# Optimization experiments

Hardware: AMD Instinct MI355X
Metric: run time of the kernel (lower is better)

The kernel has to match this reference:

```python
import jax, jax.numpy as jnp
import numpy as np

B, M, P = 128, 35, 224  # batch, num Zernike modes, pupil_size
SIGN_PENALTY = 10.0
RECON_WEIGHT = 0.4
DEFOCUS_RAD = 1.0
EPS = 1e-8


def setup_inputs() -> dict:
    key = jax.random.key(0)
    k1, k2, k3, k4 = jax.random.split(key, 4)
    pred = jax.random.normal(k1, (B, M), dtype=jnp.float32)
    target = jax.random.normal(k2, (B, M), dtype=jnp.float32)
    input_psfs = jax.random.uniform(k3, (B, 2, P, P), dtype=jnp.float32)
    zernike_basis = jax.random.normal(k4, (M, P, P), dtype=jnp.float32)
    pupil_mask = jnp.ones((P, P), dtype=jnp.float32)
    return {
        "pred": pred,
        "target": target,
        "input_psfs": input_psfs,
        "zernike_basis": zernike_basis,
        "pupil_mask": pupil_mask,
    }


def _psf_from_phase(phase, pupil_mask):
    # phase: [B,P,P] real; pupil: masked complex field
    pupil = pupil_mask[None, :, :] * jnp.exp(1j * phase)
    field = jnp.fft.fftshift(jnp.fft.fft2(pupil), axes=(-2, -1))
    psf = field.real ** 2 + field.imag ** 2  # |FFT|^2
    psf = psf / (psf.sum(axis=(-2, -1), keepdims=True) + EPS)
    return psf


def reference(pred, target, input_psfs, zernike_basis, pupil_mask):
    # --- sign-weighted MSE on Zernike coefficients ---
    base = (pred - target) ** 2
    sign_match = jnp.sign(pred) * jnp.sign(target)
    weight = jnp.where(sign_match < 0, SIGN_PENALTY, 1.0)
    z_loss = jnp.mean(base * weight)

    # --- batched differentiable PSF reconstruction loss ---
    phase = jnp.einsum('bm,mhw->bhw', pred, zernike_basis)
    phase = phase * pupil_mask[None, :, :]

    sim_if = _psf_from_phase(phase, pupil_mask)  # in-focus

    lin = jnp.linspace(-1.0, 1.0, P, dtype=jnp.float32)
    y, x = jnp.meshgrid(lin, lin, indexing='ij')
    r2 = x ** 2 + y ** 2
    defocus_phase = DEFOCUS_RAD * (2.0 * r2 - 1.0)  # [P,P]
    sim_podf = _psf_from_phase(phase + defocus_phase[None, :, :], pupil_mask)

    # per-sample F.mse_loss then mean over batch == mean over the batched arrays
    recon_loss = (jnp.mean((sim_if - input_psfs[:, 0]) ** 2)
                  + jnp.mean((sim_podf - input_psfs[:, 1]) ** 2))

    return z_loss + RECON_WEIGHT * recon_loss
```

## Files before the change

kernel.cpp:

```cpp
#include <hip/hip_runtime.h>
#include <math.h>

#define BB 128
#define MM 35
#define PSZ 224
#define PP (PSZ*PSZ)
#define SIGN_PENALTY 10.0f
#define RECON_WEIGHT 0.4f
#define DEFOCUS_RAD 1.0f
#define EPS_F 1e-8f
#define INV2PI 0.15915494309189535f


#define WS_PHASE_OFF    2048
#define WS_T_OFF        (WS_PHASE_OFF + BB*PP)
#define N_PARTIALS      (14*BB*2)
#define S1 232
#define S2 17

static constexpr float W16R[16] = {
    1.0f, 0.9238795325f, 0.7071067812f, 0.3826834324f, 0.0f,
    -0.3826834324f, -0.7071067812f, -0.9238795325f, -1.0f,
    -0.9238795325f, -0.7071067812f, -0.3826834324f, 0.0f,
    0.3826834324f, 0.7071067812f, 0.9238795325f};
static constexpr float W16I[16] = {
    0.0f, -0.3826834324f, -0.7071067812f, -0.9238795325f, -1.0f,
    -0.9238795325f, -0.7071067812f, -0.3826834324f, 0.0f,
    0.3826834324f, 0.7071067812f, 0.9238795325f, 1.0f,
    0.9238795325f, 0.7071067812f, 0.3826834324f};
static constexpr float W7R[7] = {
    1.0f, 0.6234898019f, -0.2225209340f, -0.9009688679f,
    -0.9009688679f, -0.2225209340f, 0.6234898019f};
static constexpr float W7I[7] = {
    0.0f, -0.7818314825f, -0.9749279122f, -0.4338837391f,
    0.4338837391f, 0.9749279122f, 0.7818314825f};
static constexpr float W14R[7] = {
    1.0f, 0.9009688679f, 0.6234898019f, 0.2225209340f, -0.2225209340f,
    -0.6234898019f, -0.9009688679f};
static constexpr float W14I[7] = {
    0.0f, -0.4338837391f, -0.7818314825f, -0.9749279122f, -0.9749279122f,
    -0.7818314825f, -0.4338837391f};

__device__ __forceinline__ float lincoord(int i) {
    return -1.0f + 2.0f * (float)i / (float)(PSZ - 1);
}
__device__ __forceinline__ void fast_sincos(float x, float* s, float* c) {
    float rv = x * INV2PI;
    rv -= floorf(rv);
    *s = __builtin_amdgcn_sinf(rv);
    *c = __builtin_amdgcn_cosf(rv);
}
__device__ __forceinline__ float2 wexp_neg(float frac) {
    float rv = -frac;
    rv -= floorf(rv);
    return make_float2(__builtin_amdgcn_cosf(rv), __builtin_amdgcn_sinf(rv));
}
__device__ __forceinline__ unsigned pack_bf2(float a, float b) {
    return ((__float_as_uint(a) + 0x8000u) >> 16) |
           ((__float_as_uint(b) + 0x8000u) & 0xffff0000u);
}
__device__ __forceinline__ float2 unpack_bf2(unsigned v) {
    return make_float2(__uint_as_float(v << 16), __uint_as_float(v & 0xffff0000u));
}
__device__ __forceinline__ float2 cmul(float2 a, float2 b) {
    return make_float2(fmaf(a.x, b.x, -a.y * b.y), fmaf(a.x, b.y, a.y * b.x));
}
__device__ __forceinline__ float2 cmulc(float2 a, float wr, float wi) {
    return make_float2(fmaf(a.x, wr, -a.y * wi), fmaf(a.x, wi, a.y * wr));
}
__device__ __forceinline__ float2 cadd(float2 a, float2 b) {
    return make_float2(a.x + b.x, a.y + b.y);
}
__device__ __forceinline__ float2 csub(float2 a, float2 b) {
    return make_float2(a.x - b.x, a.y - b.y);
}
__device__ __forceinline__ void cfma(float& acc, float c, float v) {
    if (c == 0.f) return;
    if (c == 1.f)  { acc += v; return; }
    if (c == -1.f) { acc -= v; return; }
    acc = fmaf(c, v, acc);
}

__device__ __forceinline__ void dft8_sym(const float2* u, float2* X) {
    float2 a1 = cadd(u[1], u[7]), b1 = csub(u[1], u[7]);
    float2 a2 = cadd(u[2], u[6]), b2 = csub(u[2], u[6]);
    float2 a3 = cadd(u[3], u[5]), b3 = csub(u[3], u[5]);
    float2 s04 = cadd(u[0], u[4]), d04 = csub(u[0], u[4]);
    X[0] = cadd(cadd(s04, a1), cadd(a2, a3));
    X[4] = cadd(csub(s04, a1), csub(a2, a3));
    {
        float2 p = csub(s04, a2);
        float2 q = csub(b1, b3);
        X[2] = make_float2(p.x + q.y, p.y - q.x);
        X[6] = make_float2(p.x - q.y, p.y + q.x);
    }
#pragma unroll
    for (int m = 1; m <= 3; m += 2) {
        float Px = d04.x, Py = d04.y, Qx = 0.f, Qy = 0.f;
#pragma unroll
        for (int n = 1; n <= 3; n++) {
            const float cR = W16R[(2 * n * m) & 15], cI = W16I[(2 * n * m) & 15];
            const float2 a = (n == 1) ? a1 : (n == 2) ? a2 : a3;
            const float2 b = (n == 1) ? b1 : (n == 2) ? b2 : b3;
            cfma(Px, cR, a.x); cfma(Py, cR, a.y);
            cfma(Qx, cI, b.x); cfma(Qy, cI, b.y);
        }
        X[m]     = make_float2(Px - Qy, Py + Qx);
        X[8 - m] = make_float2(Px + Qy, Py - Qx);
    }
}

__device__ __forceinline__ void dft7_sym(const float2* x, float2* X) {
    float2 a1 = cadd(x[1], x[6]), b1 = csub(x[1], x[6]);
    float2 a2 = cadd(x[2], x[5]), b2 = csub(x[2], x[5]);
    float2 a3 = cadd(x[3], x[4]), b3 = csub(x[3], x[4]);
    X[0] = cadd(cadd(x[0], a1), cadd(a2, a3));
#pragma unroll
    for (int k = 1; k <= 3; k++) {
        float Px = x[0].x, Py = x[0].y, Qx = 0.f, Qy = 0.f;
#pragma unroll
        for (int n = 1; n <= 3; n++) {
            const float cR = W7R[(n * k) % 7], cI = W7I[(n * k) % 7];
            const float2 a = (n == 1) ? a1 : (n == 2) ? a2 : a3;
            const float2 b = (n == 1) ? b1 : (n == 2) ? b2 : b3;
            cfma(Px, cR, a.x); cfma(Py, cR, a.y);
            cfma(Qx, cI, b.x); cfma(Qy, cI, b.y);
        }
        X[k]     = make_float2(Px - Qy, Py + Qx);
        X[7 - k] = make_float2(Px + Qy, Py - Qx);
    }
}

__device__ __forceinline__ void inner16_sym(unsigned* __restrict__ xbuf,
                                            int base, int mul, int n1) {
    float2 x[16];
#pragma unroll
    for (int n = 0; n < 16; n++) x[n] = unpack_bf2(xbuf[base + (14 * n) * mul]);
    float2 u[8], v[8];
#pragma unroll
    for (int n = 0; n < 8; n++) {
        u[n] = cadd(x[n], x[n + 8]);
        float2 w = csub(x[n], x[n + 8]);
        v[n] = (n == 0) ? w : cmulc(w, W16R[n], W16I[n]);
    }
    float2 u1w = wexp_neg((float)n1 * (1.0f / 224.0f));
    float2 u2w = wexp_neg((float)n1 * (1.0f / 112.0f));
    {
        float2 Xe[8];
        dft8_sym(u, Xe);
        float2 cur = make_float2(1.f, 0.f);
#pragma unroll
        for (int m = 0; m < 8; m++) {
            float2 z = (m == 0) ? Xe[0] : cmul(Xe[m], cur);
            xbuf[base + (14 * (2 * m)) * mul] = pack_bf2(z.x, z.y);
            cur = cmul(cur, u2w);
        }
    }
    {
        float2 Xo[8];
        dft8_sym(v, Xo);
        float2 cur = u1w;
#pragma unroll
        for (int m = 0; m < 8; m++) {
            float2 z = cmul(Xo[m], cur);
            xbuf[base + (14 * (2 * m + 1)) * mul] = pack_bf2(z.x, z.y);
            cur = cmul(cur, u2w);
        }
    }
}

__global__ __launch_bounds__(256) void k_phase(const float* __restrict__ pred,
                                               const float* __restrict__ target,
                                               const float* __restrict__ zern,
                                               const float* __restrict__ mask,
                                               float* __restrict__ phase,
                                               float* __restrict__ ws) {
    __shared__ float pl[32 * MM];
    __shared__ float red[256];
    int t = threadIdx.x;
    if (blockIdx.x == 196) {
        int y = blockIdx.y;
        float s = 0.f;
        if (y == 0) {
            for (int i = t; i < BB * MM; i += 256) {
                float p = pred[i], tg = target[i];
                float dd = p - tg;
                float w = (p * tg < 0.f) ? SIGN_PENALTY : 1.f;
                s = fmaf(dd * dd, w, s);
            }
        } else {
            const int F4 = PP / 4;
            int st = (y - 1) * 4182;
            int en = (y == 3) ? F4 : st + 4182;
            const float4* m4 = (const float4*)mask;
            for (int i = st + t; i < en; i += 256) {
                float4 v = m4[i];
                s = fmaf(v.x, v.x, s); s = fmaf(v.y, v.y, s);
                s = fmaf(v.z, v.z, s); s = fmaf(v.w, v.w, s);
            }
        }
        red[t] = s;
        __syncthreads();
        for (int st = 128; st > 0; st >>= 1) {
            if (t < st) red[t] += red[t + st];
            __syncthreads();
        }
        if (t == 0) {
            if (y == 0) ws[1] = red[0] / (float)(BB * MM);
            else        ws[1 + y] = red[0];
        }
        return;
    }
    int bg = blockIdx.y;
    for (int i = t; i < 32 * MM; i += 256) {
        int j = i / MM, m = i % MM;
        pl[i] = pred[(bg * 32 + j) * MM + m];
    }
    __syncthreads();
    int pix = blockIdx.x * 256 + t;
    float acc[32];
#pragma unroll
    for (int j = 0; j < 32; j++) acc[j] = 0.f;
    for (int m = 0; m < MM; m++) {
        float z = zern[m * PP + pix];
#pragma unroll
        for (int j = 0; j < 32; j++) acc[j] = fmaf(pl[j * MM + m], z, acc[j]);
    }
    float mk = mask[pix];
#pragma unroll
    for (int j = 0; j < 32; j++) phase[(size_t)(bg * 32 + j) * PP + pix] = acc[j] * mk;
}

__global__ __launch_bounds__(256, 6) void k_stage1(const float* __restrict__ phase,
                                                   const float* __restrict__ mask,
                                                   unsigned* __restrict__ T) {
    __shared__ unsigned xs[16 * S1];
    int h0 = blockIdx.x * 16;
    int b = blockIdx.y, d = blockIdx.z;
    int t = threadIdx.x;

    const float* ph_base = phase + (size_t)b * PP + (size_t)h0 * PSZ;
    for (int idx = t; idx < 16 * PSZ; idx += 256) {
        int r = idx / PSZ, w = idx - r * PSZ;
        float ph = ph_base[r * PSZ + w];
        if (d) {
            float vy = lincoord(h0 + r), vx = lincoord(w);
            ph += DEFOCUS_RAD * (2.f * (vx * vx + vy * vy) - 1.f);
        }
        float mk = mask[(h0 + r) * PSZ + w];
        float sn, cs;
        fast_sincos(ph, &sn, &cs);
        xs[r * S1 + w] = pack_bf2(mk * cs, mk * sn);
    }
    __syncthreads();

    if (t < 224) {
        int r = t / 14, n1 = t - r * 14;
        inner16_sym(xs, r * S1 + n1, 1, n1);
    }
    __syncthreads();

    {
        int r = t >> 4, k2 = t & 15;
        const unsigned* xr = xs + r * S1 + k2 * 14;
        int img = d * BB + b;
        unsigned* Trow = T + ((size_t)img * PSZ + (h0 + r)) * PSZ;
        float2 e[7], E[7], O[7];
#pragma unroll
        for (int n = 0; n < 7; n++) e[n] = unpack_bf2(xr[2 * n]);
        dft7_sym(e, E);
#pragma unroll
        for (int n = 0; n < 7; n++) e[n] = unpack_bf2(xr[2 * n + 1]);
        dft7_sym(e, O);
#pragma unroll
        for (int k1 = 0; k1 < 7; k1++) {
            float2 op = (k1 == 0) ? O[0] : cmulc(O[k1], W14R[k1], W14I[k1]);
            float2 s = cadd(E[k1], op), q = csub(E[k1], op);
            Trow[16 * k1 + k2]       = pack_bf2(s.x, s.y);
            Trow[16 * (k1 + 7) + k2] = pack_bf2(q.x, q.y);
        }
    }
}

__global__ __launch_bounds__(256, 6) void k_stage2(const unsigned* __restrict__ T,
                                                   const float* __restrict__ psfs,
                                                   const float* __restrict__ ws,
                                                   float* __restrict__ partials) {
    __shared__ unsigned xs[224 * S2];
    __shared__ float red[4];
    int tile = blockIdx.x, b = blockIdx.y, d = blockIdx.z;
    int img = d * BB + b;
    int col0 = tile * 16;
    int t = threadIdx.x;
    int k2o = t >> 4, c = t & 15;

    const unsigned* Tbase = T + (size_t)img * PP + col0;
    const float* inp = psfs + ((size_t)b * 2 + d) * PP;
    int scol = 16 * ((tile + 7) % 14) + c;
    float pf[14];
#pragma unroll
    for (int i = 0; i < 14; i++) {
        int idx = t + 256 * i;
        int h = idx >> 4, cc = idx & 15;
        xs[h * S2 + cc] = Tbase[(size_t)h * PSZ + cc];
    }
#pragma unroll
    for (int j = 0; j < 7; j++) {
        pf[j]     = inp[(size_t)(112 + 16 * j + k2o) * PSZ + scol];
        pf[j + 7] = inp[(size_t)(16 * j + k2o) * PSZ + scol];
    }
    __syncthreads();

    if (t < 224) {
        int n1 = t >> 4, cc = t & 15;
        inner16_sym(xs, n1 * S2 + cc, S2, n1);
    }
    __syncthreads();

    float m2 = ws[2] + ws[3] + ws[4];
    float inv_denom = 1.f / (m2 * (float)PP + EPS_F);

    float lsum = 0.f;
    {
        float2 e[7], E[7], O[7];
#pragma unroll
        for (int n = 0; n < 7; n++) e[n] = unpack_bf2(xs[(k2o * 14 + 2 * n) * S2 + c]);
        dft7_sym(e, E);
#pragma unroll
        for (int n = 0; n < 7; n++) e[n] = unpack_bf2(xs[(k2o * 14 + 2 * n + 1) * S2 + c]);
        dft7_sym(e, O);
#pragma unroll
        for (int k1 = 0; k1 < 7; k1++) {
            float2 op = (k1 == 0) ? O[0] : cmulc(O[k1], W14R[k1], W14I[k1]);
            float2 s = cadd(E[k1], op), q = csub(E[k1], op);
            float ds = fmaf(s.x, s.x, s.y * s.y) * inv_denom - pf[k1];
            float dq = fmaf(q.x, q.x, q.y * q.y) * inv_denom - pf[k1 + 7];
            lsum = fmaf(ds, ds, lsum);
            lsum = fmaf(dq, dq, lsum);
        }
    }
#pragma unroll
    for (int off = 32; off > 0; off >>= 1)
        lsum += __shfl_down(lsum, off, 64);
    if ((t & 63) == 0) red[t >> 6] = lsum;
    __syncthreads();
    if (t == 0)
        partials[(blockIdx.z * BB + blockIdx.y) * 14 + blockIdx.x] =
            red[0] + red[1] + red[2] + red[3];
}

__global__ void k_final(const float* __restrict__ ws,
                        const float* __restrict__ partials,
                        float* __restrict__ out) {
    __shared__ float red[256];
    float s = 0.f;
    for (int i = threadIdx.x; i < N_PARTIALS; i += 256) s += partials[i];
    red[threadIdx.x] = s;
    __syncthreads();
    for (int st = 128; st > 0; st >>= 1) {
        if (threadIdx.x < st) red[threadIdx.x] += red[threadIdx.x + st];
        __syncthreads();
    }
    if (threadIdx.x == 0) {
        float recon = red[0] / (float)((size_t)BB * PP);
        out[0] = ws[1] + RECON_WEIGHT * recon;
    }
}

extern "C" void kernel_launch(void* const* d_in, const int* in_sizes, int n_in,
                              void* d_out, int out_size, void* d_ws, size_t ws_size,
                              hipStream_t stream) {
    const float* pred   = (const float*)d_in[0];
    const float* target = (const float*)d_in[1];
    const float* psfs   = (const float*)d_in[2];
    const float* zern   = (const float*)d_in[3];
    const float* mask   = (const float*)d_in[4];

    float*    ws       = (float*)d_ws;
    float*    phase    = ws + WS_PHASE_OFF;
    float*    partials = ws + WS_PHASE_OFF;
    unsigned* T        = (unsigned*)(ws + WS_T_OFF);
    float*    out      = (float*)d_out;

    k_phase<<<dim3(197, 4), 256, 0, stream>>>(pred, target, zern, mask, phase, ws);
    k_stage1<<<dim3(14, BB, 2), 256, 0, stream>>>(phase, mask, T);
    k_stage2<<<dim3(14, BB, 2), 256, 0, stream>>>(T, psfs, ws, partials);
    k_final<<<1, 256, 0, stream>>>(ws, partials, out);
}
```

Before: 180.3 us.

## Fuse in-focus and defocus stage-1 FFTs, tile T layout, load stage-2 from global

Stage 1 now runs one block per (row tile, batch) and produces both the in-focus and defocused pupil fields from a single phase read. The defocus term is applied as a complex rotation by a precomputed defocus exponential rather than a second sincos on the summed phase. The intermediate T buffer is relaid into column-tiled blocks so stage 2 reads contiguous tiles and does its first radix-16 pass straight from global memory, skipping a shared-memory staging copy and one barrier. The change also swaps the bf16 pack to a hardware conversion instruction and adjusts LDS strides, at the cost of more LDS and registers per stage-1 block (occupancy hint lowered to 5).

```diff
diff --git a/kernel.cpp b/kernel.cpp
--- a/kernel.cpp
+++ b/kernel.cpp
@@ -15,8 +15,8 @@
 #define WS_PHASE_OFF    2048
 #define WS_T_OFF        (WS_PHASE_OFF + BB*PP)
 #define N_PARTIALS      (14*BB*2)
-#define S1 232
-#define S2 17
+#define S1 233
+#define S2 20
 
 static constexpr float W16R[16] = {
     1.0f, 0.9238795325f, 0.7071067812f, 0.3826834324f, 0.0f,
@@ -56,8 +56,9 @@
     return make_float2(__builtin_amdgcn_cosf(rv), __builtin_amdgcn_sinf(rv));
 }
 __device__ __forceinline__ unsigned pack_bf2(float a, float b) {
-    return ((__float_as_uint(a) + 0x8000u) >> 16) |
-           ((__float_as_uint(b) + 0x8000u) & 0xffff0000u);
+    unsigned r;
+    asm("v_cvt_pk_bf16_f32 %0, %1, %2" : "=v"(r) : "v"(a), "v"(b));
+    return r;
 }
 __device__ __forceinline__ float2 unpack_bf2(unsigned v) {
     return make_float2(__uint_as_float(v << 16), __uint_as_float(v & 0xffff0000u));
@@ -164,6 +165,47 @@
         for (int m = 0; m < 8; m++) {
             float2 z = cmul(Xo[m], cur);
             xbuf[base + (14 * (2 * m + 1)) * mul] = pack_bf2(z.x, z.y);
+            cur = cmul(cur, u2w);
+        }
+    }
+}
+
+__device__ __forceinline__ void inner16_g2l(const unsigned* __restrict__ gin,
+                                            unsigned* __restrict__ xs,
+                                            int n1, int cc) {
+    float2 x[16];
+#pragma unroll
+    for (int n = 0; n < 16; n++)
+        x[n] = unpack_bf2(gin[224 * n + 16 * n1 + cc]);
+    float2 u[8], v[8];
+#pragma unroll
+    for (int n = 0; n < 8; n++) {
+        u[n] = cadd(x[n], x[n + 8]);
+        float2 w = csub(x[n], x[n + 8]);
+        v[n] = (n == 0) ? w : cmulc(w, W16R[n], W16I[n]);
+    }
+    float2 u1w = wexp_neg((float)n1 * (1.0f / 224.0f));
+    float2 u2w = wexp_neg((float)n1 * (1.0f / 112.0f));
+    unsigned* xb = xs + n1 * S2 + cc;
+    {
+        float2 Xe[8];
+        dft8_sym(u, Xe);
+        float2 cur = make_float2(1.f, 0.f);
+#pragma unroll
+        for (int m = 0; m < 8; m++) {
+            float2 z = (m == 0) ? Xe[0] : cmul(Xe[m], cur);
+            xb[(14 * (2 * m)) * S2] = pack_bf2(z.x, z.y);
+            cur = cmul(cur, u2w);
+        }
+    }
+    {
+        float2 Xo[8];
+        dft8_sym(v, Xo);
+        float2 cur = u1w;
+#pragma unroll
+        for (int m = 0; m < 8; m++) {
+            float2 z = cmul(Xo[m], cur);
+            xb[(14 * (2 * m + 1)) * S2] = pack_bf2(z.x, z.y);
             cur = cmul(cur, u2w);
         }
     }
@@ -231,53 +273,61 @@
     for (int j = 0; j < 32; j++) phase[(size_t)(bg * 32 + j) * PP + pix] = acc[j] * mk;
 }
 
-__global__ __launch_bounds__(256, 6) void k_stage1(const float* __restrict__ phase,
+__global__ __launch_bounds__(256, 5) void k_stage1(const float* __restrict__ phase,
                                                    const float* __restrict__ mask,
                                                    unsigned* __restrict__ T) {
-    __shared__ unsigned xs[16 * S1];
+    __shared__ unsigned xs0[16 * S1];
+    __shared__ unsigned xs1[16 * S1];
     int h0 = blockIdx.x * 16;
-    int b = blockIdx.y, d = blockIdx.z;
+    int b = blockIdx.y;
     int t = threadIdx.x;
 
     const float* ph_base = phase + (size_t)b * PP + (size_t)h0 * PSZ;
     for (int idx = t; idx < 16 * PSZ; idx += 256) {
         int r = idx / PSZ, w = idx - r * PSZ;
         float ph = ph_base[r * PSZ + w];
-        if (d) {
-            float vy = lincoord(h0 + r), vx = lincoord(w);
-            ph += DEFOCUS_RAD * (2.f * (vx * vx + vy * vy) - 1.f);
-        }
         float mk = mask[(h0 + r) * PSZ + w];
         float sn, cs;
         fast_sincos(ph, &sn, &cs);
-        xs[r * S1 + w] = pack_bf2(mk * cs, mk * sn);
+        float vy = lincoord(h0 + r), vx = lincoord(w);
+        float df = DEFOCUS_RAD * (2.f * (vx * vx + vy * vy) - 1.f);
+        float sd, cd;
+        fast_sincos(df, &sd, &cd);
+        float c0 = mk * cs, s0 = mk * sn;
+        xs0[r * S1 + w] = pack_bf2(c0, s0);
+        xs1[r * S1 + w] = pack_bf2(fmaf(c0, cd, -s0 * sd),
+                                   fmaf(s0, cd,  c0 * sd));
     }
     __syncthreads();
 
     if (t < 224) {
-        int r = t / 14, n1 = t - r * 14;
-        inner16_sym(xs, r * S1 + n1, 1, n1);
+        int r = t / 14, n1 = t - (t / 14) * 14;
+        inner16_sym(xs0, r * S1 + n1, 1, n1);
+        inner16_sym(xs1, r * S1 + n1, 1, n1);
     }
     __syncthreads();
 
     {
         int r = t >> 4, k2 = t & 15;
-        const unsigned* xr = xs + r * S1 + k2 * 14;
-        int img = d * BB + b;
-        unsigned* Trow = T + ((size_t)img * PSZ + (h0 + r)) * PSZ;
-        float2 e[7], E[7], O[7];
-#pragma unroll
-        for (int n = 0; n < 7; n++) e[n] = unpack_bf2(xr[2 * n]);
-        dft7_sym(e, E);
-#pragma unroll
-        for (int n = 0; n < 7; n++) e[n] = unpack_bf2(xr[2 * n + 1]);
-        dft7_sym(e, O);
-#pragma unroll
-        for (int k1 = 0; k1 < 7; k1++) {
-            float2 op = (k1 == 0) ? O[0] : cmulc(O[k1], W14R[k1], W14I[k1]);
-            float2 s = cadd(E[k1], op), q = csub(E[k1], op);
-            Trow[16 * k1 + k2]       = pack_bf2(s.x, s.y);
-            Trow[16 * (k1 + 7) + k2] = pack_bf2(q.x, q.y);
+#pragma unroll
+        for (int dd = 0; dd < 2; dd++) {
+            const unsigned* xr = (dd ? xs1 : xs0) + r * S1 + k2 * 14;
+            int img = dd * BB + b;
+            unsigned* Tt = T + (((size_t)img * 14) * PSZ + (h0 + r)) * 16 + k2;
+            float2 e[7], E[7], O[7];
+#pragma unroll
+            for (int n = 0; n < 7; n++) e[n] = unpack_bf2(xr[2 * n]);
+            dft7_sym(e, E);
+#pragma unroll
+            for (int n = 0; n < 7; n++) e[n] = unpack_bf2(xr[2 * n + 1]);
+            dft7_sym(e, O);
+#pragma unroll
+            for (int k1 = 0; k1 < 7; k1++) {
+                float2 op = (k1 == 0) ? O[0] : cmulc(O[k1], W14R[k1], W14I[k1]);
+                float2 s = cadd(E[k1], op), q = csub(E[k1], op);
+                Tt[(size_t)k1 * (PSZ * 16)]       = pack_bf2(s.x, s.y);
+                Tt[(size_t)(k1 + 7) * (PSZ * 16)] = pack_bf2(q.x, q.y);
+            }
         }
     }
 }
@@ -290,31 +340,21 @@
     __shared__ float red[4];
     int tile = blockIdx.x, b = blockIdx.y, d = blockIdx.z;
     int img = d * BB + b;
-    int col0 = tile * 16;
     int t = threadIdx.x;
     int k2o = t >> 4, c = t & 15;
 
-    const unsigned* Tbase = T + (size_t)img * PP + col0;
+    const unsigned* Tb = T + ((size_t)img * 14 + tile) * (PSZ * 16);
     const float* inp = psfs + ((size_t)b * 2 + d) * PP;
     int scol = 16 * ((tile + 7) % 14) + c;
     float pf[14];
 #pragma unroll
-    for (int i = 0; i < 14; i++) {
-        int idx = t + 256 * i;
-        int h = idx >> 4, cc = idx & 15;
-        xs[h * S2 + cc] = Tbase[(size_t)h * PSZ + cc];
-    }
-#pragma unroll
     for (int j = 0; j < 7; j++) {
         pf[j]     = inp[(size_t)(112 + 16 * j + k2o) * PSZ + scol];
         pf[j + 7] = inp[(size_t)(16 * j + k2o) * PSZ + scol];
     }
-    __syncthreads();
-
-    if (t < 224) {
-        int n1 = t >> 4, cc = t & 15;
-        inner16_sym(xs, n1 * S2 + cc, S2, n1);
-    }
+
+    if (t < 224)
+        inner16_g2l(Tb, xs, t >> 4, t & 15);
     __syncthreads();
 
     float m2 = ws[2] + ws[3] + ws[4];
@@ -383,7 +423,7 @@
     float*    out      = (float*)d_out;
 
     k_phase<<<dim3(197, 4), 256, 0, stream>>>(pred, target, zern, mask, phase, ws);
-    k_stage1<<<dim3(14, BB, 2), 256, 0, stream>>>(phase, mask, T);
+    k_stage1<<<dim3(14, BB), 256, 0, stream>>>(phase, mask, T);
     k_stage2<<<dim3(14, BB, 2), 256, 0, stream>>>(T, psfs, ws, partials);
     k_final<<<1, 256, 0, stream>>>(ws, partials, out);
 }
```

New measurement: 168.4 us. 1.07x faster.
